# Performance work log

Measured on AMD Instinct MI355X. Metric: run time of the kernel, lower is better.

The kernel has to match this reference:

```python
import jax, jax.numpy as jnp
import numpy as np

B, S, I, H = 16, 2048, 1024, 1024

def setup_inputs() -> dict:
    key = jax.random.key(0)
    ks = jax.random.split(key, 6)
    scale_ih = 1.0 / np.sqrt(I)
    scale_hh = 1.0 / np.sqrt(H)
    return {
        "x": jax.random.normal(ks[0], (B, S, I), dtype=jnp.float32),
        "hx": jax.random.normal(ks[1], (B, H), dtype=jnp.float32),
        "W_ih": jax.random.normal(ks[2], (H, I), dtype=jnp.float32) * scale_ih,
        "W_hh": jax.random.normal(ks[3], (H, H), dtype=jnp.float32) * scale_hh,
        "b_ih": jax.random.normal(ks[4], (H,), dtype=jnp.float32) * scale_ih,
        "b_hh": jax.random.normal(ks[5], (H,), dtype=jnp.float32) * scale_hh,
    }

def reference(x, hx, W_ih, W_hh, b_ih, b_hh):
    # Faithful to RecurrentCellWrapper: the Python loop passes the SAME
    # initial hx to the cell at every timestep (hx is never updated),
    # so all steps are independent and fully vectorizable.
    # cell: h' = tanh(x_t @ W_ih^T + b_ih + hx @ W_hh^T + b_hh)
    h_term = hx @ W_hh.T + b_hh + b_ih            # [B, H], shared across steps
    x_term = jnp.einsum('bsi,hi->bsh', x, W_ih)   # [B, S, H]
    out = jnp.tanh(x_term + h_term[:, None, :])   # [B, S, H]
    # batch_first=True: output already [batch, seq, hidden]
    return out
```

## Files before the change

kernel.cpp:

```cpp
#include <hip/hip_runtime.h>
#include <hip/hip_bf16.h>
#include <stdint.h>


#define M_TOT 32768
#define N_TOT 1024
#define K_TOT 1024

typedef short short8 __attribute__((ext_vector_type(8)));
typedef float f32x4  __attribute__((ext_vector_type(4)));

#define WS_WBF_OFF 0
#define WS_HT_OFF  2097152

__device__ __forceinline__ unsigned short f32_to_bf16_rne(float f) {
    union { float f; unsigned int u; } v; v.f = f;
    unsigned int u = v.u;
    unsigned int r = u + 0x7fffu + ((u >> 16) & 1u);
    return (unsigned short)(r >> 16);
}

__device__ __forceinline__ unsigned int cvt_pk_bf16(float lo, float hi) {
    unsigned int r;
    asm("v_cvt_pk_bf16_f32 %0, %1, %2" : "=v"(r) : "v"(lo), "v"(hi));
    return r;
}

__device__ __forceinline__ float fast_tanh(float z) {
    float e = __expf(2.0f * z);
    return 1.0f - 2.0f / (e + 1.0f);
}

__global__ void prep_kernel(const float* __restrict__ hx,
                            const float* __restrict__ whh,
                            const float* __restrict__ bih,
                            const float* __restrict__ bhh,
                            const float* __restrict__ wih,
                            float* __restrict__ ht,
                            unsigned short* __restrict__ wbf) {
    if (blockIdx.x < 4096) {
        int lane = threadIdx.x & 63;
        int w    = threadIdx.x >> 6;
        int wg   = blockIdx.x * 4 + w;
        int b = wg >> 10, h = wg & 1023;
        const float* hr = hx  + (long long)b * 1024;
        const float* wr = whh + (long long)h * 1024;
        float s = 0.f;
#pragma unroll
        for (int p = 0; p < 4; ++p) {
            int idx = p * 256 + lane * 4;
            float4 a = *(const float4*)(hr + idx);
            float4 c = *(const float4*)(wr + idx);
            s += a.x * c.x + a.y * c.y + a.z * c.z + a.w * c.w;
        }
#pragma unroll
        for (int d = 32; d > 0; d >>= 1) s += __shfl_down(s, d, 64);
        if (lane == 0) ht[wg] = s + bih[h] + bhh[h];
    } else {
        int g = (blockIdx.x - 4096) * 256 + threadIdx.x;
        for (int v = g; v < 131072; v += 32768) {
            long long base = (long long)v * 8;
            float4 a = *(const float4*)(wih + base);
            float4 b = *(const float4*)(wih + base + 4);
            union { unsigned short s[8]; uint4 u; } o;
            o.s[0] = f32_to_bf16_rne(a.x); o.s[1] = f32_to_bf16_rne(a.y);
            o.s[2] = f32_to_bf16_rne(a.z); o.s[3] = f32_to_bf16_rne(a.w);
            o.s[4] = f32_to_bf16_rne(b.x); o.s[5] = f32_to_bf16_rne(b.y);
            o.s[6] = f32_to_bf16_rne(b.z); o.s[7] = f32_to_bf16_rne(b.w);
            *(uint4*)(wbf + base) = o.u;
        }
    }
}

#define GLDS16(gp, lp) \
    __builtin_amdgcn_global_load_lds((const __attribute__((address_space(1))) void*)(gp), \
                                     (__attribute__((address_space(3))) void*)(lp), 16, 0, 0)

#define KITER(T, P, CUR0, CUR1, CUR2, CUR3, NXT0, NXT1, NXT2, NXT3)            \
  {                                                                            \
              \
    const int kb = (((T) + 1) & 31) * 32;                                      \
    GLDS16(gB0 + kb, ldsB0 + ((P) ^ 1) * 16384);                               \
    GLDS16(gB1 + kb, ldsB1 + ((P) ^ 1) * 16384);                               \
    __builtin_amdgcn_sched_barrier(0);         \
                     \
    const int ka = (((T) + 2) & 31) * 32;                                      \
    NXT0 = *(const float4*)(gA + ka + 0);                                      \
    NXT1 = *(const float4*)(gA + ka + 4);                                      \
    NXT2 = *(const float4*)(gA + ka + 8);                                      \
    NXT3 = *(const float4*)(gA + ka + 12);                                     \
                                       \
    {                                                                          \
      const char* lb = lds + (P) * 16384;                                      \
      short8 af[4], bfr[4];                                                    \
      _Pragma("unroll")                                                        \
      for (int t4 = 0; t4 < 4; ++t4) {                                         \
        af[t4]  = *(const short8*)(lb + offA[t4]);                             \
        bfr[t4] = *(const short8*)(lb + offB[t4]);                             \
      }                                                                        \
      _Pragma("unroll")                                                        \
      for (int mt = 0; mt < 4; ++mt)                                           \
        _Pragma("unroll")                                                      \
        for (int nt = 0; nt < 4; ++nt)                                         \
          acc[mt][nt] = __builtin_amdgcn_mfma_f32_16x16x32_bf16(               \
              af[mt], bfr[nt], acc[mt][nt], 0, 0, 0);                          \
    }                                                                          \
         \
    {                                                                          \
      uint4 pk0, pk1;                                                          \
      pk0.x = cvt_pk_bf16(CUR0.x, CUR0.y); pk0.y = cvt_pk_bf16(CUR0.z, CUR0.w);\
      pk0.z = cvt_pk_bf16(CUR1.x, CUR1.y); pk0.w = cvt_pk_bf16(CUR1.z, CUR1.w);\
      pk1.x = cvt_pk_bf16(CUR2.x, CUR2.y); pk1.y = cvt_pk_bf16(CUR2.z, CUR2.w);\
      pk1.z = cvt_pk_bf16(CUR3.x, CUR3.y); pk1.w = cvt_pk_bf16(CUR3.z, CUR3.w);\
      *(uint4*)(lA0 + ((P) ^ 1) * 16384) = pk0;                                \
      *(uint4*)(lA1 + ((P) ^ 1) * 16384) = pk1;                                \
    }                                                                          \
                     \
    __builtin_amdgcn_sched_barrier(0);                                         \
    asm volatile("s_waitcnt vmcnt(4)" ::: "memory");                           \
    asm volatile("s_waitcnt lgkmcnt(0)" ::: "memory");                         \
    __builtin_amdgcn_s_barrier();                                              \
    __builtin_amdgcn_sched_barrier(0);                                         \
  }

__global__ __launch_bounds__(256) void gemm_tanh_kernel(
    const float* __restrict__ X,
    const unsigned short* __restrict__ Bm,
    const float* __restrict__ ht,
    float* __restrict__ out)
{
    __shared__ __align__(16) char lds[32768];

    const int tid = threadIdx.x;
    const int w = tid >> 6, l = tid & 63;

    const int bid  = blockIdx.x;
    const int widx = (bid & 7) * 256 + (bid >> 3);
    const int tile_m = widx >> 3;
    const int tile_n = widx & 7;
    const int m0 = tile_m << 7, n0 = tile_n << 7;

    const int rowA  = tid >> 1;
    const int halfA = tid & 1;
    const float* gA = X + (long long)(m0 + rowA) * K_TOT + halfA * 16;
    const int swzA = (rowA >> 1) & 3;
    char* lA0 = lds + rowA * 64 + (((halfA * 2 + 0 + swzA) & 3) << 4);
    char* lA1 = lds + rowA * 64 + (((halfA * 2 + 1 + swzA) & 3) << 4);

    const int r0 = (w * 2 + 0) * 16 + (l >> 2);
    const int r1 = (w * 2 + 1) * 16 + (l >> 2);
    const int slot = l & 3;
    const int qg0 = (slot - (r0 >> 1)) & 3;
    const int qg1 = (slot - (r1 >> 1)) & 3;
    const unsigned short* gB0 = Bm + (long long)(n0 + r0) * K_TOT + qg0 * 8;
    const unsigned short* gB1 = Bm + (long long)(n0 + r1) * K_TOT + qg1 * 8;
    char* ldsB0 = lds + 8192 + (w * 2 + 0) * 1024;
    char* ldsB1 = lds + 8192 + (w * 2 + 1) * 1024;

    const int wm = w & 1, wn = w >> 1;
    const int lm = l & 15, q = l >> 4;
    int offA[4], offB[4];
#pragma unroll
    for (int t = 0; t < 4; ++t) {
        int rr = wm * 64 + t * 16 + lm;
        offA[t] = rr * 64 + (((q + (rr >> 1)) & 3) << 4);
        int nn = wn * 64 + t * 16 + lm;
        offB[t] = 8192 + nn * 64 + (((q + (nn >> 1)) & 3) << 4);
    }

    f32x4 acc[4][4];
#pragma unroll
    for (int i = 0; i < 4; ++i)
#pragma unroll
        for (int j = 0; j < 4; ++j)
            acc[i][j] = (f32x4){0.f, 0.f, 0.f, 0.f};

    float4 s0_0, s0_1, s0_2, s0_3;
    float4 s1_0, s1_1, s1_2, s1_3;

    s0_0 = *(const float4*)(gA + 0);
    s0_1 = *(const float4*)(gA + 4);
    s0_2 = *(const float4*)(gA + 8);
    s0_3 = *(const float4*)(gA + 12);
    GLDS16(gB0, ldsB0);
    GLDS16(gB1, ldsB1);
    __builtin_amdgcn_sched_barrier(0);
    {
        uint4 pk0, pk1;
        pk0.x = cvt_pk_bf16(s0_0.x, s0_0.y); pk0.y = cvt_pk_bf16(s0_0.z, s0_0.w);
        pk0.z = cvt_pk_bf16(s0_1.x, s0_1.y); pk0.w = cvt_pk_bf16(s0_1.z, s0_1.w);
        pk1.x = cvt_pk_bf16(s0_2.x, s0_2.y); pk1.y = cvt_pk_bf16(s0_2.z, s0_2.w);
        pk1.z = cvt_pk_bf16(s0_3.x, s0_3.y); pk1.w = cvt_pk_bf16(s0_3.z, s0_3.w);
        *(uint4*)lA0 = pk0;
        *(uint4*)lA1 = pk1;
    }
    s1_0 = *(const float4*)(gA + 32 + 0);
    s1_1 = *(const float4*)(gA + 32 + 4);
    s1_2 = *(const float4*)(gA + 32 + 8);
    s1_3 = *(const float4*)(gA + 32 + 12);
    __builtin_amdgcn_sched_barrier(0);
    asm volatile("s_waitcnt vmcnt(4)" ::: "memory");
    asm volatile("s_waitcnt lgkmcnt(0)" ::: "memory");
    __builtin_amdgcn_s_barrier();
    __builtin_amdgcn_sched_barrier(0);

    for (int tt = 0; tt < 32; tt += 2) {
        KITER(tt,     0, s1_0, s1_1, s1_2, s1_3, s0_0, s0_1, s0_2, s0_3);
        KITER(tt + 1, 1, s0_0, s0_1, s0_2, s0_3, s1_0, s1_1, s1_2, s1_3);
    }
    asm volatile("s_waitcnt vmcnt(0)" ::: "memory");

    const int b = tile_m >> 4;
    float htv[4];
#pragma unroll
    for (int nt = 0; nt < 4; ++nt)
        htv[nt] = ht[b * 1024 + n0 + wn * 64 + nt * 16 + lm];

#pragma unroll
    for (int mt = 0; mt < 4; ++mt) {
#pragma unroll
        for (int nt = 0; nt < 4; ++nt) {
            int n = n0 + wn * 64 + nt * 16 + lm;
#pragma unroll
            for (int r = 0; r < 4; ++r) {
                int m = m0 + wm * 64 + mt * 16 + q * 4 + r;
                float z = acc[mt][nt][r] + htv[nt];
                out[(long long)m * N_TOT + n] = fast_tanh(z);
            }
        }
    }
}

extern "C" void kernel_launch(void* const* d_in, const int* in_sizes, int n_in,
                              void* d_out, int out_size, void* d_ws, size_t ws_size,
                              hipStream_t stream) {
    const float* x    = (const float*)d_in[0];
    const float* hx   = (const float*)d_in[1];
    const float* wih  = (const float*)d_in[2];
    const float* whh  = (const float*)d_in[3];
    const float* bih  = (const float*)d_in[4];
    const float* bhh  = (const float*)d_in[5];
    float* out = (float*)d_out;

    unsigned short* wbf = (unsigned short*)((char*)d_ws + WS_WBF_OFF);
    float*          htp = (float*)((char*)d_ws + WS_HT_OFF);

    prep_kernel<<<4224, 256, 0, stream>>>(hx, whh, bih, bhh, wih, htp, wbf);
    gemm_tanh_kernel<<<2048, 256, 0, stream>>>(x, wbf, htp, out);
}
```

Before: 361.7 us.

## Deepen GEMM pipeline to triple-buffered LDS with longer A prefetch distance

Grows LDS from two to three 16 KB stages with rotating compute and write buffer offsets. B tiles are now fetched two k-steps ahead and fp32 A registers four steps ahead. The A conversion and LDS store move before the MFMA block, and the wait is relaxed to vmcnt(10). This is meant to hide more global-load latency behind compute, at the cost of more LDS per block (which may lower occupancy) and more in-flight registers.

```diff
diff --git a/kernel.cpp b/kernel.cpp
--- a/kernel.cpp
+++ b/kernel.cpp
@@ -76,22 +76,34 @@
     __builtin_amdgcn_global_load_lds((const __attribute__((address_space(1))) void*)(gp), \
                                      (__attribute__((address_space(3))) void*)(lp), 16, 0, 0)
 
-#define KITER(T, P, CUR0, CUR1, CUR2, CUR3, NXT0, NXT1, NXT2, NXT3)            \
+#define KITER(T, CUR0, CUR1, CUR2, CUR3)                                       \
   {                                                                            \
-              \
-    const int kb = (((T) + 1) & 31) * 32;                                      \
-    GLDS16(gB0 + kb, ldsB0 + ((P) ^ 1) * 16384);                               \
-    GLDS16(gB1 + kb, ldsB1 + ((P) ^ 1) * 16384);                               \
-    __builtin_amdgcn_sched_barrier(0);         \
-                     \
-    const int ka = (((T) + 2) & 31) * 32;                                      \
-    NXT0 = *(const float4*)(gA + ka + 0);                                      \
-    NXT1 = *(const float4*)(gA + ka + 4);                                      \
-    NXT2 = *(const float4*)(gA + ka + 8);                                      \
-    NXT3 = *(const float4*)(gA + ka + 12);                                     \
-                                       \
+            \
+    const int kb = (((T) + 2) & 31) * 32;                                      \
+    GLDS16(gB0 + kb, ldsB0 + bufW);                                            \
+    GLDS16(gB1 + kb, ldsB1 + bufW);                                            \
+    __builtin_amdgcn_sched_barrier(0);                                         \
+        \
     {                                                                          \
-      const char* lb = lds + (P) * 16384;                                      \
+      uint4 pk0, pk1;                                                          \
+      pk0.x = cvt_pk_bf16(CUR0.x, CUR0.y); pk0.y = cvt_pk_bf16(CUR0.z, CUR0.w);\
+      pk0.z = cvt_pk_bf16(CUR1.x, CUR1.y); pk0.w = cvt_pk_bf16(CUR1.z, CUR1.w);\
+      pk1.x = cvt_pk_bf16(CUR2.x, CUR2.y); pk1.y = cvt_pk_bf16(CUR2.z, CUR2.w);\
+      pk1.z = cvt_pk_bf16(CUR3.x, CUR3.y); pk1.w = cvt_pk_bf16(CUR3.z, CUR3.w);\
+      *(uint4*)(lA0 + bufW) = pk0;                                             \
+      *(uint4*)(lA1 + bufW) = pk1;                                             \
+    }                                                                          \
+    __builtin_amdgcn_sched_barrier(0);                                         \
+               \
+    const int ka = (((T) + 4) & 31) * 32;                                      \
+    CUR0 = *(const float4*)(gA + ka + 0);                                      \
+    CUR1 = *(const float4*)(gA + ka + 4);                                      \
+    CUR2 = *(const float4*)(gA + ka + 8);                                      \
+    CUR3 = *(const float4*)(gA + ka + 12);                                     \
+    __builtin_amdgcn_sched_barrier(0);                                         \
+                                     \
+    {                                                                          \
+      const char* lb = lds + bufC;                                             \
       short8 af[4], bfr[4];                                                    \
       _Pragma("unroll")                                                        \
       for (int t4 = 0; t4 < 4; ++t4) {                                         \
@@ -105,22 +117,14 @@
           acc[mt][nt] = __builtin_amdgcn_mfma_f32_16x16x32_bf16(               \
               af[mt], bfr[nt], acc[mt][nt], 0, 0, 0);                          \
     }                                                                          \
-         \
-    {                                                                          \
-      uint4 pk0, pk1;                                                          \
-      pk0.x = cvt_pk_bf16(CUR0.x, CUR0.y); pk0.y = cvt_pk_bf16(CUR0.z, CUR0.w);\
-      pk0.z = cvt_pk_bf16(CUR1.x, CUR1.y); pk0.w = cvt_pk_bf16(CUR1.z, CUR1.w);\
-      pk1.x = cvt_pk_bf16(CUR2.x, CUR2.y); pk1.y = cvt_pk_bf16(CUR2.z, CUR2.w);\
-      pk1.z = cvt_pk_bf16(CUR3.x, CUR3.y); pk1.w = cvt_pk_bf16(CUR3.z, CUR3.w);\
-      *(uint4*)(lA0 + ((P) ^ 1) * 16384) = pk0;                                \
-      *(uint4*)(lA1 + ((P) ^ 1) * 16384) = pk1;                                \
-    }                                                                          \
-                     \
-    __builtin_amdgcn_sched_barrier(0);                                         \
-    asm volatile("s_waitcnt vmcnt(4)" ::: "memory");                           \
+    \
+    __builtin_amdgcn_sched_barrier(0);                                         \
+    asm volatile("s_waitcnt vmcnt(10)" ::: "memory");                          \
     asm volatile("s_waitcnt lgkmcnt(0)" ::: "memory");                         \
     __builtin_amdgcn_s_barrier();                                              \
     __builtin_amdgcn_sched_barrier(0);                                         \
+    bufC = (bufC == 32768) ? 0 : bufC + 16384;                                 \
+    bufW = (bufW == 32768) ? 0 : bufW + 16384;                                 \
   }
 
 __global__ __launch_bounds__(256) void gemm_tanh_kernel(
@@ -129,7 +133,7 @@
     const float* __restrict__ ht,
     float* __restrict__ out)
 {
-    __shared__ __align__(16) char lds[32768];
+    __shared__ __align__(16) char lds[49152];
 
     const int tid = threadIdx.x;
     const int w = tid >> 6, l = tid & 63;
@@ -175,38 +179,48 @@
         for (int j = 0; j < 4; ++j)
             acc[i][j] = (f32x4){0.f, 0.f, 0.f, 0.f};
 
-    float4 s0_0, s0_1, s0_2, s0_3;
-    float4 s1_0, s1_1, s1_2, s1_3;
-
-    s0_0 = *(const float4*)(gA + 0);
-    s0_1 = *(const float4*)(gA + 4);
-    s0_2 = *(const float4*)(gA + 8);
-    s0_3 = *(const float4*)(gA + 12);
-    GLDS16(gB0, ldsB0);
-    GLDS16(gB1, ldsB1);
-    __builtin_amdgcn_sched_barrier(0);
+    float4 e0, e1, e2, e3;
+    float4 o0, o1, o2, o3;
+
+    GLDS16(gB0 +  0, ldsB0);         GLDS16(gB1 +  0, ldsB1);
+    GLDS16(gB0 + 32, ldsB0 + 16384); GLDS16(gB1 + 32, ldsB1 + 16384);
+    __builtin_amdgcn_sched_barrier(0);
+    e0 = *(const float4*)(gA + 0);  e1 = *(const float4*)(gA + 4);
+    e2 = *(const float4*)(gA + 8);  e3 = *(const float4*)(gA + 12);
     {
         uint4 pk0, pk1;
-        pk0.x = cvt_pk_bf16(s0_0.x, s0_0.y); pk0.y = cvt_pk_bf16(s0_0.z, s0_0.w);
-        pk0.z = cvt_pk_bf16(s0_1.x, s0_1.y); pk0.w = cvt_pk_bf16(s0_1.z, s0_1.w);
-        pk1.x = cvt_pk_bf16(s0_2.x, s0_2.y); pk1.y = cvt_pk_bf16(s0_2.z, s0_2.w);
-        pk1.z = cvt_pk_bf16(s0_3.x, s0_3.y); pk1.w = cvt_pk_bf16(s0_3.z, s0_3.w);
-        *(uint4*)lA0 = pk0;
-        *(uint4*)lA1 = pk1;
-    }
-    s1_0 = *(const float4*)(gA + 32 + 0);
-    s1_1 = *(const float4*)(gA + 32 + 4);
-    s1_2 = *(const float4*)(gA + 32 + 8);
-    s1_3 = *(const float4*)(gA + 32 + 12);
-    __builtin_amdgcn_sched_barrier(0);
-    asm volatile("s_waitcnt vmcnt(4)" ::: "memory");
+        pk0.x = cvt_pk_bf16(e0.x, e0.y); pk0.y = cvt_pk_bf16(e0.z, e0.w);
+        pk0.z = cvt_pk_bf16(e1.x, e1.y); pk0.w = cvt_pk_bf16(e1.z, e1.w);
+        pk1.x = cvt_pk_bf16(e2.x, e2.y); pk1.y = cvt_pk_bf16(e2.z, e2.w);
+        pk1.z = cvt_pk_bf16(e3.x, e3.y); pk1.w = cvt_pk_bf16(e3.z, e3.w);
+        *(uint4*)lA0 = pk0;  *(uint4*)lA1 = pk1;
+    }
+    o0 = *(const float4*)(gA + 32); o1 = *(const float4*)(gA + 36);
+    o2 = *(const float4*)(gA + 40); o3 = *(const float4*)(gA + 44);
+    {
+        uint4 pk0, pk1;
+        pk0.x = cvt_pk_bf16(o0.x, o0.y); pk0.y = cvt_pk_bf16(o0.z, o0.w);
+        pk0.z = cvt_pk_bf16(o1.x, o1.y); pk0.w = cvt_pk_bf16(o1.z, o1.w);
+        pk1.x = cvt_pk_bf16(o2.x, o2.y); pk1.y = cvt_pk_bf16(o2.z, o2.w);
+        pk1.z = cvt_pk_bf16(o3.x, o3.y); pk1.w = cvt_pk_bf16(o3.z, o3.w);
+        *(uint4*)(lA0 + 16384) = pk0;  *(uint4*)(lA1 + 16384) = pk1;
+    }
+    __builtin_amdgcn_sched_barrier(0);
+    e0 = *(const float4*)(gA + 64); e1 = *(const float4*)(gA + 68);
+    e2 = *(const float4*)(gA + 72); e3 = *(const float4*)(gA + 76);
+    o0 = *(const float4*)(gA + 96); o1 = *(const float4*)(gA + 100);
+    o2 = *(const float4*)(gA + 104); o3 = *(const float4*)(gA + 108);
+    __builtin_amdgcn_sched_barrier(0);
     asm volatile("s_waitcnt lgkmcnt(0)" ::: "memory");
     __builtin_amdgcn_s_barrier();
     __builtin_amdgcn_sched_barrier(0);
 
+    int bufC = 0;
+    int bufW = 32768;
+
     for (int tt = 0; tt < 32; tt += 2) {
-        KITER(tt,     0, s1_0, s1_1, s1_2, s1_3, s0_0, s0_1, s0_2, s0_3);
-        KITER(tt + 1, 1, s0_0, s0_1, s0_2, s0_3, s1_0, s1_1, s1_2, s1_3);
+        KITER(tt,     e0, e1, e2, e3);
+        KITER(tt + 1, o0, o1, o2, o3);
     }
     asm volatile("s_waitcnt vmcnt(0)" ::: "memory");
 
```

Result: slower. 385.6 us (+6.6%).
